# Performance work log

Hardware: AMD Instinct MI355X
Metric: run time of the kernel (lower is better)

Reference implementation:

```python
import jax, jax.numpy as jnp
import numpy as np

N = 50000      # nodes
E = 800000     # edges (avg degree 16)
D_IN = 64
D_OUT = 64


def setup_inputs() -> dict:
    key = jax.random.key(0)
    k1, k2, k3 = jax.random.split(key, 3)
    x = jax.random.normal(k1, (N, D_IN), dtype=jnp.float32)
    edge_index = jax.random.randint(k2, (2, E), 0, N, dtype=jnp.int32)
    W = jax.random.normal(k3, (D_OUT, D_IN), dtype=jnp.float32) * 0.05
    b = jnp.zeros((D_OUT,), dtype=jnp.float32)
    prelu_a = jnp.full((1,), 0.25, dtype=jnp.float32)  # nn.PReLU() default
    return {"x": x, "edge_index": edge_index, "W": W, "b": b, "prelu_a": prelu_a}


def reference(x, edge_index, W, b, prelu_a):
    # GCNConv (PyG, normalize=True, add_self_loops=True) + PReLU.
    # Dropout is identity at inference and omitted.
    n = x.shape[0]
    row, col = edge_index[0], edge_index[1]
    loop = jnp.arange(n, dtype=edge_index.dtype)
    row = jnp.concatenate([row, loop])  # [E+N] source nodes
    col = jnp.concatenate([col, loop])  # [E+N] target nodes

    # Symmetric degree normalization: deg over targets (edge weight = 1).
    ones = jnp.ones(row.shape[0], dtype=x.dtype)
    deg = jax.ops.segment_sum(ones, col, num_segments=n)          # [N]
    dinv = jnp.where(deg > 0, jax.lax.rsqrt(deg), 0.0)            # deg^{-1/2}
    norm = dinv[row] * dinv[col]                                  # [E+N]

    h = x @ W.T                                                   # [N, D_OUT]
    msg = h[row] * norm[:, None]                                  # gather + scale
    out = jax.ops.segment_sum(msg, col, num_segments=n) + b       # scatter-add

    # PReLU with a single shared slope parameter
    return jnp.where(out >= 0, out, prelu_a * out)
```

## Files before the change

kernel.cpp:

```cpp
#include <hip/hip_runtime.h>
#include <hip/hip_bf16.h>

#define D 64
#define CAP 64
#define GROUPS 8
#define GEMM_BLOCKS 2048
#define ZERO_BLOCKS 49

typedef float f32x4 __attribute__((ext_vector_type(4)));

__device__ __forceinline__ float bflo(unsigned u) {
    union { unsigned i; float f; } x; x.i = u << 16; return x.f;
}
__device__ __forceinline__ float bfhi(unsigned u) {
    union { unsigned i; float f; } x; x.i = u & 0xffff0000u; return x.f;
}

__global__ void __launch_bounds__(256) gemm_zero_kernel(
    const float* __restrict__ x, const float* __restrict__ W,
    unsigned short* __restrict__ h, int4* __restrict__ cnt4, int nzero4, int n)
{
    if (blockIdx.x < ZERO_BLOCKS) {
        int i = blockIdx.x * 256 + threadIdx.x;
        if (i < nzero4) cnt4[i] = make_int4(0, 0, 0, 0);
    }

    __shared__ float Ws[D * 65];
    __shared__ float xs[4][D];

    int tid = threadIdx.x;
    #pragma unroll
    for (int k = 0; k < 16; ++k) {
        int idx = tid + k * 256;
        Ws[(idx >> 6) * 65 + (idx & 63)] = W[idx];
    }

    int ln = tid >> 6;
    int o  = tid & 63;
    int nquad = (n + 3) >> 2;
    for (int q = blockIdx.x; q < nquad; q += GEMM_BLOCKS) {
        int node = q * 4 + ln;
        __syncthreads();
        if (node < n) xs[ln][o] = x[(size_t)node * D + o];
        __syncthreads();
        if (node < n) {
            float sum = 0.0f;
            #pragma unroll
            for (int i = 0; i < D; ++i) sum += xs[ln][i] * Ws[o * 65 + i];
            __hip_bfloat16 hb = __float2bfloat16(sum);
            unsigned short us;
            __builtin_memcpy(&us, &hb, 2);
            __builtin_nontemporal_store(us, &h[(size_t)node * D + o]);
        }
    }
}

__global__ void __launch_bounds__(256) fill_kernel(
    const int* __restrict__ row, const int* __restrict__ col,
    const int4* __restrict__ row4, const int4* __restrict__ col4,
    int* __restrict__ cnt, unsigned short* __restrict__ srcs,
    int* __restrict__ ovf_cnt, int2* __restrict__ ovf, int E, int E4, int n)
{
    int g   = blockIdx.x & (GROUPS - 1);
    int bg  = blockIdx.x >> 3;
    int bpg = gridDim.x >> 3;
    int npg = (n + GROUPS - 1) / GROUPS;
    int lo  = g * npg;
    int hi  = lo + npg < n ? lo + npg : n;
    int stride = bpg * 256;

    for (int i = bg * 256 + threadIdx.x; i < E4; i += stride) {
        int4 cc = col4[i];
        int4 rr = row4[i];
        #pragma unroll
        for (int j = 0; j < 4; ++j) {
            int c = (j == 0) ? cc.x : (j == 1) ? cc.y : (j == 2) ? cc.z : cc.w;
            int r = (j == 0) ? rr.x : (j == 1) ? rr.y : (j == 2) ? rr.z : rr.w;
            if (c >= lo && c < hi) {
                int slot = atomicAdd(&cnt[c], 1);
                if (slot < CAP) {
                    srcs[(size_t)c * CAP + slot] = (unsigned short)r;
                } else {
                    int oi = atomicAdd(ovf_cnt, 1);
                    ovf[oi] = make_int2(r, c);
                }
            }
        }
    }
    for (int e = E4 * 4 + bg * 256 + threadIdx.x; e < E; e += stride) {
        int c = col[e];
        if (c >= lo && c < hi) {
            int r = row[e];
            int slot = atomicAdd(&cnt[c], 1);
            if (slot < CAP) {
                srcs[(size_t)c * CAP + slot] = (unsigned short)r;
            } else {
                int oi = atomicAdd(ovf_cnt, 1);
                ovf[oi] = make_int2(r, c);
            }
        }
    }
}

__global__ void __launch_bounds__(256) gather_kernel(
    const int* __restrict__ cnt, const unsigned short* __restrict__ srcs,
    const unsigned short* __restrict__ h,
    const float* __restrict__ b, const float* __restrict__ prelu_a,
    const int* __restrict__ ovf_cnt, const int2* __restrict__ ovf,
    float* __restrict__ out, int n)
{
    int grp = blockIdx.x & (GROUPS - 1);
    int bg  = blockIdx.x >> 3;
    int bpg = gridDim.x >> 3;
    int npg = (n + GROUPS - 1) / GROUPS;
    int lo  = grp * npg;
    int hi  = lo + npg < n ? lo + npg : n;

    int tid  = threadIdx.x;
    int lane = tid & 63;
    int wig  = bg * 4 + (tid >> 6);
    int wpg  = bpg * 4;
    int g    = lane >> 3;
    int q    = lane & 7;

    for (int c = lo + wig; c < hi; c += wpg) {
        int deg = cnt[c];
        int m = deg < CAP ? deg : CAP;
        float dc = rsqrtf((float)deg + 1.0f);

        int   s  = 0;
        float wl = 0.0f;
        if (lane < m) {
            s  = (int)srcs[(size_t)c * CAP + lane];
            wl = rsqrtf((float)cnt[s] + 1.0f) * dc;
        }

        float acc[8] = {0.f, 0.f, 0.f, 0.f, 0.f, 0.f, 0.f, 0.f};
        int m8 = (m + 7) & ~7;
        for (int k = 0; k < m8; k += 8) {
            int   sk = __shfl(s,  k + g);
            float wk = __shfl(wl, k + g);
            uint4 v = *reinterpret_cast<const uint4*>(&h[(size_t)sk * D + q * 8]);
            acc[0] += wk * bflo(v.x);  acc[1] += wk * bfhi(v.x);
            acc[2] += wk * bflo(v.y);  acc[3] += wk * bfhi(v.y);
            acc[4] += wk * bflo(v.z);  acc[5] += wk * bfhi(v.z);
            acc[6] += wk * bflo(v.w);  acc[7] += wk * bfhi(v.w);
        }

        #pragma unroll
        for (int j = 0; j < 8; ++j) {
            acc[j] += __shfl_xor(acc[j], 8);
            acc[j] += __shfl_xor(acc[j], 16);
            acc[j] += __shfl_xor(acc[j], 32);
        }

        if (g == 0) {
            uint4 hv = *reinterpret_cast<const uint4*>(&h[(size_t)c * D + q * 8]);
            float dc2 = dc * dc;
            float hc[8] = { bflo(hv.x), bfhi(hv.x), bflo(hv.y), bfhi(hv.y),
                            bflo(hv.z), bfhi(hv.z), bflo(hv.w), bfhi(hv.w) };
            #pragma unroll
            for (int j = 0; j < 8; ++j) {
                acc[j] += hc[j] * dc2 + b[q * 8 + j];
            }

            int nov = *ovf_cnt;
            for (int i = 0; i < nov; ++i) {
                int2 rc = ovf[i];
                if (rc.y == c) {
                    float wo = rsqrtf((float)cnt[rc.x] + 1.0f) * dc;
                    uint4 ov = *reinterpret_cast<const uint4*>(&h[(size_t)rc.x * D + q * 8]);
                    acc[0] += wo * bflo(ov.x);  acc[1] += wo * bfhi(ov.x);
                    acc[2] += wo * bflo(ov.y);  acc[3] += wo * bfhi(ov.y);
                    acc[4] += wo * bflo(ov.z);  acc[5] += wo * bfhi(ov.z);
                    acc[6] += wo * bflo(ov.w);  acc[7] += wo * bfhi(ov.w);
                }
            }

            float al = prelu_a[0];
            #pragma unroll
            for (int j = 0; j < 8; ++j) {
                acc[j] = acc[j] >= 0.0f ? acc[j] : al * acc[j];
            }
            f32x4 o0 = { acc[0], acc[1], acc[2], acc[3] };
            f32x4 o1 = { acc[4], acc[5], acc[6], acc[7] };
            f32x4* op = (f32x4*)&out[(size_t)c * D + q * 8];
            __builtin_nontemporal_store(o0, op);
            __builtin_nontemporal_store(o1, op + 1);
        }
    }
}

extern "C" void kernel_launch(void* const* d_in, const int* in_sizes, int n_in,
                              void* d_out, int out_size, void* d_ws, size_t ws_size,
                              hipStream_t stream) {
    const float* x       = (const float*)d_in[0];
    const int*   eidx    = (const int*)d_in[1];
    const float* W       = (const float*)d_in[2];
    const float* b       = (const float*)d_in[3];
    const float* prelu_a = (const float*)d_in[4];

    const int E = in_sizes[1] / 2;
    const int n = in_sizes[0] / D;
    const int* row = eidx;
    const int* col = eidx + E;

    float* out = (float*)d_out;

    int E4 = 0;
    if ((E % 4) == 0 &&
        ((uintptr_t)row % 16) == 0 && ((uintptr_t)col % 16) == 0) {
        E4 = E / 4;
    }

    unsigned short* h    = (unsigned short*)d_ws;
    unsigned short* srcs = h + (size_t)n * D;
    int*   cnt     = (int*)(srcs + (size_t)n * CAP);
    int*   ovf_cnt = cnt + n;
    int2*  ovf     = (int2*)(cnt + n + 2);

    int nzero4 = (n + 1 + 3) / 4;

    gemm_zero_kernel<<<GEMM_BLOCKS, 256, 0, stream>>>(
        x, W, h, (int4*)cnt, nzero4, n);

    fill_kernel<<<2048, 256, 0, stream>>>(
        row, col, (const int4*)row, (const int4*)col,
        cnt, srcs, ovf_cnt, ovf, E, E4, n);

    gather_kernel<<<12504, 256, 0, stream>>>(
        cnt, srcs, h, b, prelu_a, ovf_cnt, ovf, out, n);
}
```

Baseline: 92.86 us.

## Fuse GEMM and edge-bucketing fill into one launch; zero counters via memset

The separate GEMM and fill kernels are merged into one launch whose first block range does the edge bucketing and second range does the dense x@W^T, so the two independent stages can run at the same time on the GPU. Counter zeroing moves from inside the GEMM kernel to a hipMemsetAsync issued before the launch, since the fill now needs zeroed counters at its start. The aim is to save one kernel launch gap and overlap the atomic-bound fill with the compute-bound GEMM. In exchange it adds a memset operation, and the merged kernel reserves the GEMM's shared memory for every block, which may limit occupancy for the fill blocks.

```diff
diff --git a/kernel.cpp b/kernel.cpp
--- a/kernel.cpp
+++ b/kernel.cpp
@@ -4,8 +4,8 @@
 #define D 64
 #define CAP 64
 #define GROUPS 8
+#define FILL_BLOCKS 2048
 #define GEMM_BLOCKS 2048
-#define ZERO_BLOCKS 49
 
 typedef float f32x4 __attribute__((ext_vector_type(4)));
 
@@ -16,67 +16,46 @@
     union { unsigned i; float f; } x; x.i = u & 0xffff0000u; return x.f;
 }
 
-__global__ void __launch_bounds__(256) gemm_zero_kernel(
+__global__ void __launch_bounds__(256) gemmfill_kernel(
     const float* __restrict__ x, const float* __restrict__ W,
-    unsigned short* __restrict__ h, int4* __restrict__ cnt4, int nzero4, int n)
-{
-    if (blockIdx.x < ZERO_BLOCKS) {
-        int i = blockIdx.x * 256 + threadIdx.x;
-        if (i < nzero4) cnt4[i] = make_int4(0, 0, 0, 0);
-    }
-
-    __shared__ float Ws[D * 65];
-    __shared__ float xs[4][D];
-
-    int tid = threadIdx.x;
-    #pragma unroll
-    for (int k = 0; k < 16; ++k) {
-        int idx = tid + k * 256;
-        Ws[(idx >> 6) * 65 + (idx & 63)] = W[idx];
-    }
-
-    int ln = tid >> 6;
-    int o  = tid & 63;
-    int nquad = (n + 3) >> 2;
-    for (int q = blockIdx.x; q < nquad; q += GEMM_BLOCKS) {
-        int node = q * 4 + ln;
-        __syncthreads();
-        if (node < n) xs[ln][o] = x[(size_t)node * D + o];
-        __syncthreads();
-        if (node < n) {
-            float sum = 0.0f;
-            #pragma unroll
-            for (int i = 0; i < D; ++i) sum += xs[ln][i] * Ws[o * 65 + i];
-            __hip_bfloat16 hb = __float2bfloat16(sum);
-            unsigned short us;
-            __builtin_memcpy(&us, &hb, 2);
-            __builtin_nontemporal_store(us, &h[(size_t)node * D + o]);
-        }
-    }
-}
-
-__global__ void __launch_bounds__(256) fill_kernel(
     const int* __restrict__ row, const int* __restrict__ col,
     const int4* __restrict__ row4, const int4* __restrict__ col4,
-    int* __restrict__ cnt, unsigned short* __restrict__ srcs,
+    unsigned short* __restrict__ h, int* __restrict__ cnt,
+    unsigned short* __restrict__ srcs,
     int* __restrict__ ovf_cnt, int2* __restrict__ ovf, int E, int E4, int n)
 {
-    int g   = blockIdx.x & (GROUPS - 1);
-    int bg  = blockIdx.x >> 3;
-    int bpg = gridDim.x >> 3;
-    int npg = (n + GROUPS - 1) / GROUPS;
-    int lo  = g * npg;
-    int hi  = lo + npg < n ? lo + npg : n;
-    int stride = bpg * 256;
-
-    for (int i = bg * 256 + threadIdx.x; i < E4; i += stride) {
-        int4 cc = col4[i];
-        int4 rr = row4[i];
-        #pragma unroll
-        for (int j = 0; j < 4; ++j) {
-            int c = (j == 0) ? cc.x : (j == 1) ? cc.y : (j == 2) ? cc.z : cc.w;
-            int r = (j == 0) ? rr.x : (j == 1) ? rr.y : (j == 2) ? rr.z : rr.w;
+    if (blockIdx.x < FILL_BLOCKS) {
+        int bid = blockIdx.x;
+        int g   = bid & (GROUPS - 1);
+        int bg  = bid >> 3;
+        int bpg = FILL_BLOCKS >> 3;
+        int npg = (n + GROUPS - 1) / GROUPS;
+        int lo  = g * npg;
+        int hi  = lo + npg < n ? lo + npg : n;
+        int stride = bpg * 256;
+
+        for (int i = bg * 256 + threadIdx.x; i < E4; i += stride) {
+            int4 cc = col4[i];
+            int4 rr = row4[i];
+            #pragma unroll
+            for (int j = 0; j < 4; ++j) {
+                int c = (j == 0) ? cc.x : (j == 1) ? cc.y : (j == 2) ? cc.z : cc.w;
+                int r = (j == 0) ? rr.x : (j == 1) ? rr.y : (j == 2) ? rr.z : rr.w;
+                if (c >= lo && c < hi) {
+                    int slot = atomicAdd(&cnt[c], 1);
+                    if (slot < CAP) {
+                        srcs[(size_t)c * CAP + slot] = (unsigned short)r;
+                    } else {
+                        int oi = atomicAdd(ovf_cnt, 1);
+                        ovf[oi] = make_int2(r, c);
+                    }
+                }
+            }
+        }
+        for (int e = E4 * 4 + bg * 256 + threadIdx.x; e < E; e += stride) {
+            int c = col[e];
             if (c >= lo && c < hi) {
+                int r = row[e];
                 int slot = atomicAdd(&cnt[c], 1);
                 if (slot < CAP) {
                     srcs[(size_t)c * CAP + slot] = (unsigned short)r;
@@ -86,17 +65,34 @@
                 }
             }
         }
-    }
-    for (int e = E4 * 4 + bg * 256 + threadIdx.x; e < E; e += stride) {
-        int c = col[e];
-        if (c >= lo && c < hi) {
-            int r = row[e];
-            int slot = atomicAdd(&cnt[c], 1);
-            if (slot < CAP) {
-                srcs[(size_t)c * CAP + slot] = (unsigned short)r;
-            } else {
-                int oi = atomicAdd(ovf_cnt, 1);
-                ovf[oi] = make_int2(r, c);
+    } else {
+        int bid = blockIdx.x - FILL_BLOCKS;
+        __shared__ float Ws[D * 65];
+        __shared__ float xs[4][D];
+
+        int tid = threadIdx.x;
+        #pragma unroll
+        for (int k = 0; k < 16; ++k) {
+            int idx = tid + k * 256;
+            Ws[(idx >> 6) * 65 + (idx & 63)] = W[idx];
+        }
+
+        int ln = tid >> 6;
+        int o  = tid & 63;
+        int nquad = (n + 3) >> 2;
+        for (int q = bid; q < nquad; q += GEMM_BLOCKS) {
+            int node = q * 4 + ln;
+            __syncthreads();
+            if (node < n) xs[ln][o] = x[(size_t)node * D + o];
+            __syncthreads();
+            if (node < n) {
+                float sum = 0.0f;
+                #pragma unroll
+                for (int i = 0; i < D; ++i) sum += xs[ln][i] * Ws[o * 65 + i];
+                __hip_bfloat16 hb = __float2bfloat16(sum);
+                unsigned short us;
+                __builtin_memcpy(&us, &hb, 2);
+                __builtin_nontemporal_store(us, &h[(size_t)node * D + o]);
             }
         }
     }
@@ -219,14 +215,11 @@
     int*   ovf_cnt = cnt + n;
     int2*  ovf     = (int2*)(cnt + n + 2);
 
-    int nzero4 = (n + 1 + 3) / 4;
-
-    gemm_zero_kernel<<<GEMM_BLOCKS, 256, 0, stream>>>(
-        x, W, h, (int4*)cnt, nzero4, n);
-
-    fill_kernel<<<2048, 256, 0, stream>>>(
-        row, col, (const int4*)row, (const int4*)col,
-        cnt, srcs, ovf_cnt, ovf, E, E4, n);
+    hipMemsetAsync(cnt, 0, (size_t)(n + 1) * sizeof(int), stream);
+
+    gemmfill_kernel<<<FILL_BLOCKS + GEMM_BLOCKS, 256, 0, stream>>>(
+        x, W, row, col, (const int4*)row, (const int4*)col,
+        h, cnt, srcs, ovf_cnt, ovf, E, E4, n);
 
     gather_kernel<<<12504, 256, 0, stream>>>(
         cnt, srcs, h, b, prelu_a, ovf_cnt, ovf, out, n);
```

New measurement: 95.08 us. +2.4%, slower.

## Split edge bucketing into group partition pass then per-group slot fill

Applied to the files above, without the earlier changes.

The single fill kernel is replaced by two passes. The first partitions edges into one compacted buffer per node group, using a wave prefix scan and one atomic per block to reserve space. The second reads each group's compact buffer and performs the per-node atomic slot fill. Previously every group's blocks scanned all edges; now each fill block touches only its group's edges, localising the cnt atomics. The cost is an extra kernel launch and an extra write and read of a packed edge buffer, plus per-iteration block barriers.

```diff
diff --git a/kernel.cpp b/kernel.cpp
--- a/kernel.cpp
+++ b/kernel.cpp
@@ -55,11 +55,11 @@
     }
 }
 
-__global__ void __launch_bounds__(256) fill_kernel(
+__global__ void __launch_bounds__(256) partA_kernel(
     const int* __restrict__ row, const int* __restrict__ col,
     const int4* __restrict__ row4, const int4* __restrict__ col4,
-    int* __restrict__ cnt, unsigned short* __restrict__ srcs,
-    int* __restrict__ ovf_cnt, int2* __restrict__ ovf, int E, int E4, int n)
+    unsigned int* __restrict__ buf, int* __restrict__ cursors,
+    int E, int E4, int n)
 {
     int g   = blockIdx.x & (GROUPS - 1);
     int bg  = blockIdx.x >> 3;
@@ -67,37 +67,95 @@
     int npg = (n + GROUPS - 1) / GROUPS;
     int lo  = g * npg;
     int hi  = lo + npg < n ? lo + npg : n;
+    unsigned int* mybuf = buf + (size_t)g * E;
+
+    __shared__ int warp_base[4];
+    __shared__ int block_base;
+
+    int tid  = threadIdx.x;
+    int lane = tid & 63;
+    int wid  = tid >> 6;
     int stride = bpg * 256;
-
-    for (int i = bg * 256 + threadIdx.x; i < E4; i += stride) {
-        int4 cc = col4[i];
-        int4 rr = row4[i];
+    int nIter  = (E4 + stride - 1) / stride;
+
+    for (int it = 0; it < nIter; ++it) {
+        int i = it * stride + bg * 256 + tid;
+        unsigned int v0 = 0, v1 = 0, v2 = 0, v3 = 0;
+        int cl = 0;
+        if (i < E4) {
+            int4 cc = col4[i];
+            int4 rr = row4[i];
+            #pragma unroll
+            for (int j = 0; j < 4; ++j) {
+                int c = (j == 0) ? cc.x : (j == 1) ? cc.y : (j == 2) ? cc.z : cc.w;
+                int r = (j == 0) ? rr.x : (j == 1) ? rr.y : (j == 2) ? rr.z : rr.w;
+                if (c >= lo && c < hi) {
+                    unsigned int pv = ((unsigned int)(c - lo) << 16) | (unsigned int)r;
+                    if      (cl == 0) v0 = pv;
+                    else if (cl == 1) v1 = pv;
+                    else if (cl == 2) v2 = pv;
+                    else              v3 = pv;
+                    ++cl;
+                }
+            }
+        }
+        int pfx = cl;
         #pragma unroll
-        for (int j = 0; j < 4; ++j) {
-            int c = (j == 0) ? cc.x : (j == 1) ? cc.y : (j == 2) ? cc.z : cc.w;
-            int r = (j == 0) ? rr.x : (j == 1) ? rr.y : (j == 2) ? rr.z : rr.w;
-            if (c >= lo && c < hi) {
-                int slot = atomicAdd(&cnt[c], 1);
-                if (slot < CAP) {
-                    srcs[(size_t)c * CAP + slot] = (unsigned short)r;
-                } else {
-                    int oi = atomicAdd(ovf_cnt, 1);
-                    ovf[oi] = make_int2(r, c);
-                }
-            }
-        }
-    }
-    for (int e = E4 * 4 + bg * 256 + threadIdx.x; e < E; e += stride) {
+        for (int off = 1; off < 64; off <<= 1) {
+            int t = __shfl_up(pfx, off);
+            if (lane >= off) pfx += t;
+        }
+        if (lane == 63) warp_base[wid] = pfx;
+        __syncthreads();
+        if (tid == 0) {
+            int s = 0;
+            #pragma unroll
+            for (int k = 0; k < 4; ++k) { int t = warp_base[k]; warp_base[k] = s; s += t; }
+            block_base = atomicAdd(&cursors[g], s);
+        }
+        __syncthreads();
+        int myoff = block_base + warp_base[wid] + (pfx - cl);
+        if (cl > 0) mybuf[myoff]     = v0;
+        if (cl > 1) mybuf[myoff + 1] = v1;
+        if (cl > 2) mybuf[myoff + 2] = v2;
+        if (cl > 3) mybuf[myoff + 3] = v3;
+        __syncthreads();
+    }
+
+    for (int e = E4 * 4 + bg * 256 + tid; e < E; e += stride) {
         int c = col[e];
         if (c >= lo && c < hi) {
             int r = row[e];
-            int slot = atomicAdd(&cnt[c], 1);
-            if (slot < CAP) {
-                srcs[(size_t)c * CAP + slot] = (unsigned short)r;
-            } else {
-                int oi = atomicAdd(ovf_cnt, 1);
-                ovf[oi] = make_int2(r, c);
-            }
+            int pos = atomicAdd(&cursors[g], 1);
+            mybuf[pos] = ((unsigned int)(c - lo) << 16) | (unsigned int)r;
+        }
+    }
+}
+
+__global__ void __launch_bounds__(256) partB_kernel(
+    const unsigned int* __restrict__ buf, const int* __restrict__ cursors,
+    int* __restrict__ cnt, unsigned short* __restrict__ srcs,
+    int* __restrict__ ovf_cnt, int2* __restrict__ ovf, int E, int n)
+{
+    int g   = blockIdx.x & (GROUPS - 1);
+    int bg  = blockIdx.x >> 3;
+    int bpg = gridDim.x >> 3;
+    int npg = (n + GROUPS - 1) / GROUPS;
+    int lo  = g * npg;
+    const unsigned int* mybuf = buf + (size_t)g * E;
+
+    int m = cursors[g];
+    int stride = bpg * 256;
+    for (int i = bg * 256 + threadIdx.x; i < m; i += stride) {
+        unsigned int v = mybuf[i];
+        int c = lo + (int)(v >> 16);
+        int r = (int)(v & 0xFFFFu);
+        int slot = atomicAdd(&cnt[c], 1);
+        if (slot < CAP) {
+            srcs[(size_t)c * CAP + slot] = (unsigned short)r;
+        } else {
+            int oi = atomicAdd(ovf_cnt, 1);
+            ovf[oi] = make_int2(r, c);
         }
     }
 }
@@ -217,16 +275,21 @@
     unsigned short* srcs = h + (size_t)n * D;
     int*   cnt     = (int*)(srcs + (size_t)n * CAP);
     int*   ovf_cnt = cnt + n;
-    int2*  ovf     = (int2*)(cnt + n + 2);
-
-    int nzero4 = (n + 1 + 3) / 4;
+    int*   cursors = cnt + n + 1;
+    int2*  ovf     = (int2*)(cnt + n + 12);
+    unsigned int* buf = (unsigned int*)(ovf + E);
+
+    int nzero4 = (n + 12 + 3) / 4;
 
     gemm_zero_kernel<<<GEMM_BLOCKS, 256, 0, stream>>>(
         x, W, h, (int4*)cnt, nzero4, n);
 
-    fill_kernel<<<2048, 256, 0, stream>>>(
+    partA_kernel<<<2048, 256, 0, stream>>>(
         row, col, (const int4*)row, (const int4*)col,
-        cnt, srcs, ovf_cnt, ovf, E, E4, n);
+        buf, cursors, E, E4, n);
+
+    partB_kernel<<<2048, 256, 0, stream>>>(
+        buf, cursors, cnt, srcs, ovf_cnt, ovf, E, n);
 
     gather_kernel<<<12504, 256, 0, stream>>>(
         cnt, srcs, h, b, prelu_a, ovf_cnt, ovf, out, n);
```

After: 188.2 us. +102.7%, slower.

## Bucket edges by target group then build adjacency with LDS counters

Applied to the files above, without the earlier changes.

Replaces the single fill pass, in which every block scanned all edges and did global atomics on per-node counters, with a two-phase scheme. A bucket kernel partitions edges into 8 target-group buffers as packed (local col, row) words, using per-block shared histograms and one global cursor atomic per group. An insert kernel then has each of 512 blocks scan its group's buffer and count only its node window with shared-memory atomics before writing cnt. This removes the zeroing pass and the contended global atomics, at the cost of an extra launch, an E-sized staging buffer and redundant rereads of each group's buffer by 64 sub-blocks.

```diff
diff --git a/kernel.cpp b/kernel.cpp
--- a/kernel.cpp
+++ b/kernel.cpp
@@ -5,7 +5,8 @@
 #define CAP 64
 #define GROUPS 8
 #define GEMM_BLOCKS 2048
-#define ZERO_BLOCKS 49
+#define SUBB 64
+#define NPB_MAX 128
 
 typedef float f32x4 __attribute__((ext_vector_type(4)));
 
@@ -16,14 +17,18 @@
     union { unsigned i; float f; } x; x.i = u & 0xffff0000u; return x.f;
 }
 
+__device__ __forceinline__ int grp_of(int c, int npg) {
+    int g = 0;
+    #pragma unroll
+    for (int k = 1; k < 8; ++k) g += (c >= k * npg) ? 1 : 0;
+    return g;
+}
+
 __global__ void __launch_bounds__(256) gemm_zero_kernel(
     const float* __restrict__ x, const float* __restrict__ W,
-    unsigned short* __restrict__ h, int4* __restrict__ cnt4, int nzero4, int n)
+    unsigned short* __restrict__ h, int* __restrict__ zdst, int n)
 {
-    if (blockIdx.x < ZERO_BLOCKS) {
-        int i = blockIdx.x * 256 + threadIdx.x;
-        if (i < nzero4) cnt4[i] = make_int4(0, 0, 0, 0);
-    }
+    if (blockIdx.x == 0 && threadIdx.x < 12) zdst[threadIdx.x] = 0;
 
     __shared__ float Ws[D * 65];
     __shared__ float xs[4][D];
@@ -55,50 +60,116 @@
     }
 }
 
-__global__ void __launch_bounds__(256) fill_kernel(
+__global__ void __launch_bounds__(256) bucket_kernel(
     const int* __restrict__ row, const int* __restrict__ col,
     const int4* __restrict__ row4, const int4* __restrict__ col4,
-    int* __restrict__ cnt, unsigned short* __restrict__ srcs,
-    int* __restrict__ ovf_cnt, int2* __restrict__ ovf, int E, int E4, int n)
+    unsigned int* __restrict__ buf, int* __restrict__ cursors,
+    int E, int E4, int n, int npg)
 {
-    int g   = blockIdx.x & (GROUPS - 1);
-    int bg  = blockIdx.x >> 3;
-    int bpg = gridDim.x >> 3;
-    int npg = (n + GROUPS - 1) / GROUPS;
-    int lo  = g * npg;
-    int hi  = lo + npg < n ? lo + npg : n;
-    int stride = bpg * 256;
-
-    for (int i = bg * 256 + threadIdx.x; i < E4; i += stride) {
+    __shared__ int hist8[8];
+    __shared__ int base8[8];
+    int tid = threadIdx.x;
+    if (tid < 8) hist8[tid] = 0;
+    __syncthreads();
+
+    int i = blockIdx.x * 256 + tid;
+    int c0 = -1, c1 = -1, c2 = -1, c3 = -1;
+    int r0 = 0,  r1 = 0,  r2 = 0,  r3 = 0;
+    if (i < E4) {
         int4 cc = col4[i];
         int4 rr = row4[i];
+        c0 = cc.x; c1 = cc.y; c2 = cc.z; c3 = cc.w;
+        r0 = rr.x; r1 = rr.y; r2 = rr.z; r3 = rr.w;
+    }
+    int g0 = 0, g1 = 0, g2 = 0, g3 = 0;
+    int s0 = 0, s1 = 0, s2 = 0, s3 = 0;
+    if (c0 >= 0) { g0 = grp_of(c0, npg); s0 = atomicAdd(&hist8[g0], 1); }
+    if (c1 >= 0) { g1 = grp_of(c1, npg); s1 = atomicAdd(&hist8[g1], 1); }
+    if (c2 >= 0) { g2 = grp_of(c2, npg); s2 = atomicAdd(&hist8[g2], 1); }
+    if (c3 >= 0) { g3 = grp_of(c3, npg); s3 = atomicAdd(&hist8[g3], 1); }
+    __syncthreads();
+    if (tid < 8) base8[tid] = atomicAdd(&cursors[tid], hist8[tid]);
+    __syncthreads();
+    if (c0 >= 0) buf[(size_t)g0 * E + base8[g0] + s0] =
+        ((unsigned int)(c0 - g0 * npg) << 16) | (unsigned int)r0;
+    if (c1 >= 0) buf[(size_t)g1 * E + base8[g1] + s1] =
+        ((unsigned int)(c1 - g1 * npg) << 16) | (unsigned int)r1;
+    if (c2 >= 0) buf[(size_t)g2 * E + base8[g2] + s2] =
+        ((unsigned int)(c2 - g2 * npg) << 16) | (unsigned int)r2;
+    if (c3 >= 0) buf[(size_t)g3 * E + base8[g3] + s3] =
+        ((unsigned int)(c3 - g3 * npg) << 16) | (unsigned int)r3;
+
+    if (blockIdx.x == 0) {
+        for (int e = E4 * 4 + tid; e < E; e += 256) {
+            int c = col[e];
+            int r = row[e];
+            int g = grp_of(c, npg);
+            int pos = atomicAdd(&cursors[g], 1);
+            buf[(size_t)g * E + pos] = ((unsigned int)(c - g * npg) << 16) | (unsigned int)r;
+        }
+    }
+}
+
+__global__ void __launch_bounds__(256) insert_kernel(
+    const unsigned int* __restrict__ buf, const int* __restrict__ cursors,
+    int* __restrict__ cnt, unsigned short* __restrict__ srcs,
+    int* __restrict__ ovf_cnt, int2* __restrict__ ovf,
+    int E, int n, int npg, int npb)
+{
+    __shared__ int lcur[NPB_MAX];
+    int tid = threadIdx.x;
+    if (tid < NPB_MAX) lcur[tid] = 0;
+    __syncthreads();
+
+    int g  = blockIdx.x & (GROUPS - 1);
+    int sb = blockIdx.x >> 3;
+    int wlo = sb * npb;
+    int whi = wlo + npb < npg ? wlo + npb : npg;
+    int nodebase = g * npg;
+
+    const unsigned int* mybuf = buf + (size_t)g * E;
+    int m  = cursors[g];
+    int m4 = m >> 2;
+
+    const uint4* mybuf4 = (const uint4*)mybuf;
+    for (int i = tid; i < m4; i += 256) {
+        uint4 v4 = mybuf4[i];
         #pragma unroll
         for (int j = 0; j < 4; ++j) {
-            int c = (j == 0) ? cc.x : (j == 1) ? cc.y : (j == 2) ? cc.z : cc.w;
-            int r = (j == 0) ? rr.x : (j == 1) ? rr.y : (j == 2) ? rr.z : rr.w;
-            if (c >= lo && c < hi) {
-                int slot = atomicAdd(&cnt[c], 1);
+            unsigned int v = (j == 0) ? v4.x : (j == 1) ? v4.y : (j == 2) ? v4.z : v4.w;
+            int cl = (int)(v >> 16);
+            if (cl >= wlo && cl < whi) {
+                int slot = atomicAdd(&lcur[cl - wlo], 1);
                 if (slot < CAP) {
-                    srcs[(size_t)c * CAP + slot] = (unsigned short)r;
+                    srcs[(size_t)(nodebase + cl) * CAP + slot] =
+                        (unsigned short)(v & 0xFFFFu);
                 } else {
                     int oi = atomicAdd(ovf_cnt, 1);
-                    ovf[oi] = make_int2(r, c);
+                    ovf[oi] = make_int2((int)(v & 0xFFFFu), nodebase + cl);
                 }
             }
         }
     }
-    for (int e = E4 * 4 + bg * 256 + threadIdx.x; e < E; e += stride) {
-        int c = col[e];
-        if (c >= lo && c < hi) {
-            int r = row[e];
-            int slot = atomicAdd(&cnt[c], 1);
+    for (int i = m4 * 4 + tid; i < m; i += 256) {
+        unsigned int v = mybuf[i];
+        int cl = (int)(v >> 16);
+        if (cl >= wlo && cl < whi) {
+            int slot = atomicAdd(&lcur[cl - wlo], 1);
             if (slot < CAP) {
-                srcs[(size_t)c * CAP + slot] = (unsigned short)r;
+                srcs[(size_t)(nodebase + cl) * CAP + slot] =
+                    (unsigned short)(v & 0xFFFFu);
             } else {
                 int oi = atomicAdd(ovf_cnt, 1);
-                ovf[oi] = make_int2(r, c);
-            }
-        }
+                ovf[oi] = make_int2((int)(v & 0xFFFFu), nodebase + cl);
+            }
+        }
+    }
+    __syncthreads();
+
+    for (int t = tid; t < npb; t += 256) {
+        int cl = wlo + t;
+        int node = nodebase + cl;
+        if (cl < npg && node < n) cnt[node] = lcur[t];
     }
 }
 
@@ -202,6 +273,8 @@
 
     const int E = in_sizes[1] / 2;
     const int n = in_sizes[0] / D;
+    const int npg = (n + GROUPS - 1) / GROUPS;
+    const int npb = (npg + SUBB - 1) / SUBB;
     const int* row = eidx;
     const int* col = eidx + E;
 
@@ -217,16 +290,19 @@
     unsigned short* srcs = h + (size_t)n * D;
     int*   cnt     = (int*)(srcs + (size_t)n * CAP);
     int*   ovf_cnt = cnt + n;
-    int2*  ovf     = (int2*)(cnt + n + 2);
-
-    int nzero4 = (n + 1 + 3) / 4;
-
-    gemm_zero_kernel<<<GEMM_BLOCKS, 256, 0, stream>>>(
-        x, W, h, (int4*)cnt, nzero4, n);
-
-    fill_kernel<<<2048, 256, 0, stream>>>(
+    int*   cursors = cnt + n + 1;
+    int2*  ovf     = (int2*)(cnt + n + 12);
+    unsigned int* buf = (unsigned int*)(ovf + E);
+
+    gemm_zero_kernel<<<GEMM_BLOCKS, 256, 0, stream>>>(x, W, h, ovf_cnt, n);
+
+    int bblocks = E4 > 0 ? (E4 + 255) / 256 : 1;
+    bucket_kernel<<<bblocks, 256, 0, stream>>>(
         row, col, (const int4*)row, (const int4*)col,
-        cnt, srcs, ovf_cnt, ovf, E, E4, n);
+        buf, cursors, E, E4, n, npg);
+
+    insert_kernel<<<GROUPS * SUBB, 256, 0, stream>>>(
+        buf, cursors, cnt, srcs, ovf_cnt, ovf, E, n, npg, npb);
 
     gather_kernel<<<12504, 256, 0, stream>>>(
         cnt, srcs, h, b, prelu_a, ovf_cnt, ovf, out, n);
```

New measurement: 115.4 us. 24.2% more time.
